# Performance work log

Measured on AMD Instinct MI355X. Metric: run time of the kernel, lower is better.

## Reference

```python
import jax, jax.numpy as jnp
import numpy as np

N_SRC = 100000
N_DST = 20000
N_EDGES = 640000
D_IN = 128
D_OUT = 128


def setup_inputs() -> dict:
    key = jax.random.key(0)
    ks = jax.random.split(key, 6)
    feat_src = jax.random.normal(ks[0], (N_SRC, D_IN), dtype=jnp.float32)
    feat_dst = jax.random.normal(ks[1], (N_DST, D_IN), dtype=jnp.float32)
    src_idx = jax.random.randint(ks[2], (N_EDGES,), 0, N_SRC, dtype=jnp.int64 if jax.config.jax_enable_x64 else jnp.int32)
    dst_idx = jax.random.randint(ks[3], (N_EDGES,), 0, N_DST, dtype=jnp.int64 if jax.config.jax_enable_x64 else jnp.int32)
    # xavier-uniform-ish init scale for [out, in] Linear weights
    lim = float(np.sqrt(6.0 / (D_IN + D_OUT)))
    W_self = jax.random.uniform(ks[4], (D_OUT, D_IN), jnp.float32, -lim, lim)
    W_neigh = jax.random.uniform(ks[5], (D_OUT, D_IN), jnp.float32, -lim, lim)
    b_self = jnp.zeros((D_OUT,), jnp.float32)
    b_neigh = jnp.zeros((D_OUT,), jnp.float32)
    return {
        "feat_src": feat_src, "feat_dst": feat_dst,
        "src_idx": src_idx, "dst_idx": dst_idx,
        "W_self": W_self, "b_self": b_self,
        "W_neigh": W_neigh, "b_neigh": b_neigh,
    }


def reference(feat_src, feat_dst, src_idx, dst_idx, W_self, b_self, W_neigh, b_neigh):
    n_dst = feat_dst.shape[0]
    # message passing: copy_src + mean reduce over incoming edges per dst node
    msgs = feat_src[src_idx]                                   # [E, D_in]
    summed = jax.ops.segment_sum(msgs, dst_idx, num_segments=n_dst)  # [N_dst, D_in]
    deg = jax.ops.segment_sum(jnp.ones((src_idx.shape[0],), feat_src.dtype),
                              dst_idx, num_segments=n_dst)     # [N_dst]
    h_neigh = summed / jnp.maximum(deg, 1.0)[:, None]          # mean (0 for isolated)
    # rst = fc_self(h_self) + fc_neigh(h_neigh); no activation
    rst = (feat_dst @ W_self.T + b_self) + (h_neigh @ W_neigh.T + b_neigh)
    return rst
```

## Files before the change

### kernel.cpp

```cpp
#include <hip/hip_runtime.h>

#define D 128
#define NDST 20000
#define NB 256
#define CAP 96

typedef __attribute__((ext_vector_type(8))) short short8;
typedef __attribute__((ext_vector_type(4))) float f32x4;

__device__ __forceinline__ unsigned f2bf(float f) {
  unsigned x = __float_as_uint(f);
  return (x + 0x7FFFu + ((x >> 16) & 1u)) >> 16;
}
__device__ __forceinline__ unsigned pack2(float a, float b) {
  return f2bf(a) | (f2bf(b) << 16);
}
__device__ __forceinline__ float bflo(unsigned u) { return __uint_as_float(u << 16); }
__device__ __forceinline__ float bfhi(unsigned u) { return __uint_as_float(u & 0xFFFF0000u); }

__global__ __launch_bounds__(512) void p1(
    const int* __restrict__ dst_idx,
    unsigned short* __restrict__ blockHist,
    const float* __restrict__ W_self, const float* __restrict__ W_neigh,
    unsigned short* __restrict__ Wcat,
    unsigned short* __restrict__ fsrc_b,
    int n_src, int n_edges, int EPB)
{
  __shared__ unsigned int hist[NDST];
  const int tid = threadIdx.x;
  const int bid = blockIdx.x;

  if (bid < NB) {
    for (int i = tid; i < NDST / 4; i += 512)
      reinterpret_cast<uint4*>(hist)[i] = make_uint4(0u, 0u, 0u, 0u);
    __syncthreads();
    const int e0 = bid * EPB;
    const int e1 = min(e0 + EPB, n_edges);
    for (int e = e0 + tid; e < e1; e += 512)
      atomicAdd(&hist[dst_idx[e]], 1u);
    __syncthreads();
    unsigned int* rowp =
        reinterpret_cast<unsigned int*>(blockHist + (size_t)bid * NDST);
    for (int i = tid; i < NDST / 2; i += 512) {
      unsigned lo = hist[2 * i], hi = hist[2 * i + 1];
      rowp[i] = (lo & 0xFFFFu) | (hi << 16);
    }
  } else {
    int u = (bid - NB) * 512 + tid;
    const int UW = 32768 / 8;
    if (u < UW) {
      int l = u * 8;
      int n = l >> 8;
      int k0 = l & 255;
      const float* src = (k0 < D) ? (W_self + n * D + k0)
                                  : (W_neigh + n * D + (k0 - D));
      const float4* p = reinterpret_cast<const float4*>(src);
      float4 a = p[0], b = p[1];
      uint4 o;
      o.x = pack2(a.x, a.y); o.y = pack2(a.z, a.w);
      o.z = pack2(b.x, b.y); o.w = pack2(b.z, b.w);
      *reinterpret_cast<uint4*>(Wcat + (size_t)n * 256 + k0) = o;
    } else if (u < UW + D / 8) {
      int q = u - UW;
      *reinterpret_cast<uint4*>(fsrc_b + (size_t)n_src * D + q * 8) =
          make_uint4(0u, 0u, 0u, 0u);
    }
  }
}

__global__ __launch_bounds__(256) void p2conv(
    const float* __restrict__ feat_src,
    unsigned short* __restrict__ fsrc_b,
    unsigned short* __restrict__ blockHist,
    int* __restrict__ degi,
    int n_src, int n_dst, int NPB, int NCB)
{
  const int bid = blockIdx.x;
  const int tid = threadIdx.x;
  if (bid < NPB) {
    int d = bid * 256 + tid;
    if (d < n_dst) {
      unsigned run = 0;
      unsigned short* col = blockHist + d;
      #pragma unroll 8
      for (int b = 0; b < NB; ++b) {
        unsigned h = col[(size_t)b * NDST];
        col[(size_t)b * NDST] = (unsigned short)run;
        run += h;
      }
      degi[d] = (int)run;
    }
  } else {
    const long long NU = (long long)n_src * 16;
    const long long stride = (long long)NCB * 256;
    long long u = (long long)(bid - NPB) * 256 + tid;
    for (; u < NU; u += stride) {
      long long e = u * 8;
      const float4* p = reinterpret_cast<const float4*>(feat_src + e);
      float4 a = p[0], b = p[1];
      uint4 o;
      o.x = pack2(a.x, a.y); o.y = pack2(a.z, a.w);
      o.z = pack2(b.x, b.y); o.w = pack2(b.z, b.w);
      *reinterpret_cast<uint4*>(fsrc_b + e) = o;
    }
  }
}

__global__ __launch_bounds__(512) void p3(
    const int* __restrict__ src_idx,
    const int* __restrict__ dst_idx,
    const unsigned short* __restrict__ blockBase,
    int* __restrict__ bucket,
    int n_edges, int EPB)
{
  __shared__ unsigned int cur[NDST];
  const int tid = threadIdx.x;
  const int bid = blockIdx.x;
  const unsigned int* rowp =
      reinterpret_cast<const unsigned int*>(blockBase + (size_t)bid * NDST);
  for (int i = tid; i < NDST / 2; i += 512) {
    unsigned v = rowp[i];
    cur[2 * i]     = v & 0xFFFFu;
    cur[2 * i + 1] = v >> 16;
  }
  __syncthreads();
  const int e0 = bid * EPB;
  const int e1 = min(e0 + EPB, n_edges);
  for (int e = e0 + tid; e < e1; e += 512) {
    int d = dst_idx[e];
    int s = src_idx[e];
    unsigned r = atomicAdd(&cur[d], 1u);
    if (r < CAP) bucket[(size_t)d * CAP + r] = s;
  }
}

__global__ __launch_bounds__(512) void fused_tail(
    const unsigned short* __restrict__ fsrc_b,
    const int* __restrict__ degi,
    const int* __restrict__ bucket,
    const float* __restrict__ feat_dst,
    const unsigned short* __restrict__ Wcat,
    const float* __restrict__ b_self,
    const float* __restrict__ b_neigh,
    float* __restrict__ out,
    int n_src, int n_dst)
{
  __shared__ unsigned short Af[32][136];
  __shared__ unsigned short Ah[32][136];
  __shared__ unsigned short Bs[128][136];

  const int tid  = threadIdx.x;
  const int w    = tid >> 6;
  const int lane = tid & 63;
  const int row0 = blockIdx.x * 32;

  {
    int r = tid >> 4;
    int q = tid & 15;
    int gr = row0 + r;
    uint4 o = make_uint4(0u, 0u, 0u, 0u);
    if (gr < n_dst) {
      const float4* p = reinterpret_cast<const float4*>(
          feat_dst + (size_t)gr * D + q * 8);
      float4 a = p[0], b = p[1];
      o.x = pack2(a.x, a.y); o.y = pack2(a.z, a.w);
      o.z = pack2(b.x, b.y); o.w = pack2(b.z, b.w);
    }
    *reinterpret_cast<uint4*>(&Af[r][q * 8]) = o;
  }

  {
    const int g = lane >> 4;
    const int c = lane & 15;
    const uint4* fs4 = reinterpret_cast<const uint4*>(fsrc_b);

    for (int it = 0; it < 4; ++it) {
      int row = w * 4 + it;
      int gr = row0 + row;
      if (gr >= n_dst) {
        if (lane < 16)
          *reinterpret_cast<uint4*>(&Ah[row][c * 8]) = make_uint4(0u,0u,0u,0u);
        continue;
      }
      const int total = degi[gr];
      const int use = min(total, CAP);
      const int* brow = bucket + (size_t)gr * CAP;

      float acc[8];
      #pragma unroll
      for (int j = 0; j < 8; ++j) acc[j] = 0.f;

      for (int i = g; i < use; i += 16) {
        int s0 = brow[i];
        int s1 = (i + 4  < use) ? brow[i + 4]  : n_src;
        int s2 = (i + 8  < use) ? brow[i + 8]  : n_src;
        int s3 = (i + 12 < use) ? brow[i + 12] : n_src;
        uint4 v0 = fs4[(size_t)s0 * 16 + c];
        uint4 v1 = fs4[(size_t)s1 * 16 + c];
        uint4 v2 = fs4[(size_t)s2 * 16 + c];
        uint4 v3 = fs4[(size_t)s3 * 16 + c];
        acc[0] += bflo(v0.x); acc[1] += bfhi(v0.x); acc[2] += bflo(v0.y); acc[3] += bfhi(v0.y);
        acc[4] += bflo(v0.z); acc[5] += bfhi(v0.z); acc[6] += bflo(v0.w); acc[7] += bfhi(v0.w);
        acc[0] += bflo(v1.x); acc[1] += bfhi(v1.x); acc[2] += bflo(v1.y); acc[3] += bfhi(v1.y);
        acc[4] += bflo(v1.z); acc[5] += bfhi(v1.z); acc[6] += bflo(v1.w); acc[7] += bfhi(v1.w);
        acc[0] += bflo(v2.x); acc[1] += bfhi(v2.x); acc[2] += bflo(v2.y); acc[3] += bfhi(v2.y);
        acc[4] += bflo(v2.z); acc[5] += bfhi(v2.z); acc[6] += bflo(v2.w); acc[7] += bfhi(v2.w);
        acc[0] += bflo(v3.x); acc[1] += bfhi(v3.x); acc[2] += bflo(v3.y); acc[3] += bfhi(v3.y);
        acc[4] += bflo(v3.z); acc[5] += bfhi(v3.z); acc[6] += bflo(v3.w); acc[7] += bfhi(v3.w);
      }

      #pragma unroll
      for (int j = 0; j < 8; ++j) {
        acc[j] += __shfl_xor(acc[j], 16);
        acc[j] += __shfl_xor(acc[j], 32);
      }

      if (lane < 16) {
        float inv = 1.0f / fmaxf((float)total, 1.0f);
        uint4 o;
        o.x = pack2(acc[0] * inv, acc[1] * inv);
        o.y = pack2(acc[2] * inv, acc[3] * inv);
        o.z = pack2(acc[4] * inv, acc[5] * inv);
        o.w = pack2(acc[6] * inv, acc[7] * inv);
        *reinterpret_cast<uint4*>(&Ah[row][c * 8]) = o;
      }
    }
  }

  const int m  = w & 1;
  const int n0 = (w >> 1) * 2;
  const int ar = m * 16 + (lane & 15);
  const int kb = (lane >> 4) * 8;

  f32x4 acc2[2];
  acc2[0] = (f32x4){0.f, 0.f, 0.f, 0.f};
  acc2[1] = (f32x4){0.f, 0.f, 0.f, 0.f};

  #pragma unroll
  for (int kc = 0; kc < 2; ++kc) {
    __syncthreads();
    {
      int n = tid >> 2;
      int q = tid & 3;
      const uint4* p = reinterpret_cast<const uint4*>(
          Wcat + (size_t)n * 256 + kc * 128 + q * 32);
      uint4 v0 = p[0], v1 = p[1], v2 = p[2], v3 = p[3];
      *reinterpret_cast<uint4*>(&Bs[n][q * 32 + 0])  = v0;
      *reinterpret_cast<uint4*>(&Bs[n][q * 32 + 8])  = v1;
      *reinterpret_cast<uint4*>(&Bs[n][q * 32 + 16]) = v2;
      *reinterpret_cast<uint4*>(&Bs[n][q * 32 + 24]) = v3;
    }
    __syncthreads();

    const unsigned short (*Asrc)[136] = (kc == 0) ? Af : Ah;
    #pragma unroll
    for (int kh = 0; kh < 4; ++kh) {
      short8 a = *reinterpret_cast<const short8*>(&Asrc[ar][kh * 32 + kb]);
      #pragma unroll
      for (int t2 = 0; t2 < 2; ++t2) {
        short8 b = *reinterpret_cast<const short8*>(
            &Bs[(n0 + t2) * 16 + (lane & 15)][kh * 32 + kb]);
        acc2[t2] = __builtin_amdgcn_mfma_f32_16x16x32_bf16(a, b, acc2[t2], 0, 0, 0);
      }
    }
  }

  const int r0 = row0 + m * 16 + (lane >> 4) * 4;
  #pragma unroll
  for (int t2 = 0; t2 < 2; ++t2) {
    int col = (n0 + t2) * 16 + (lane & 15);
    float bv = b_self[col] + b_neigh[col];
    #pragma unroll
    for (int r = 0; r < 4; ++r) {
      int gr = r0 + r;
      if (gr < n_dst) out[(size_t)gr * D + col] = acc2[t2][r] + bv;
    }
  }
}

extern "C" void kernel_launch(void* const* d_in, const int* in_sizes, int n_in,
                              void* d_out, int out_size, void* d_ws, size_t ws_size,
                              hipStream_t stream) {
  const float* feat_src = (const float*)d_in[0];
  const float* feat_dst = (const float*)d_in[1];
  const int*   src_idx  = (const int*)d_in[2];
  const int*   dst_idx  = (const int*)d_in[3];
  const float* W_self   = (const float*)d_in[4];
  const float* b_self   = (const float*)d_in[5];
  const float* W_neigh  = (const float*)d_in[6];
  const float* b_neigh  = (const float*)d_in[7];
  float* out = (float*)d_out;

  const int n_src   = in_sizes[0] / D;
  const int n_dst   = in_sizes[1] / D;
  const int n_edges = in_sizes[2];

  unsigned short* fsrc_b = (unsigned short*)d_ws;
  unsigned short* Wcat   = fsrc_b + (size_t)(n_src + 1) * D;
  int* degi   = (int*)(Wcat + 128 * 256);
  int* bucket = degi + NDST;
  unsigned short* blockHist = (unsigned short*)(bucket + (size_t)NDST * CAP);

  const int EPB = (n_edges + NB - 1) / NB;
  const int extra = (32768 / 8 + D / 8 + 511) / 512;

  p1<<<NB + extra, 512, 0, stream>>>(
      dst_idx, blockHist, W_self, W_neigh, Wcat, fsrc_b, n_src, n_edges, EPB);

  const int NPB = (n_dst + 255) / 256;
  const int NCB = 512;
  p2conv<<<NPB + NCB, 256, 0, stream>>>(
      feat_src, fsrc_b, blockHist, degi, n_src, n_dst, NPB, NCB);

  p3<<<NB, 512, 0, stream>>>(
      src_idx, dst_idx, blockHist, bucket, n_edges, EPB);

  fused_tail<<<(n_dst + 31) / 32, 512, 0, stream>>>(
      fsrc_b, degi, bucket, feat_dst, Wcat, b_self, b_neigh, out,
      n_src, n_dst);
}
```

Baseline: 74.29 us.

## Store gathered source features as FP8 and pack histograms into 16-bit LDS halves

Converts feat_src to FP8 (e4m3) instead of bf16, which halves the bytes gathered per edge in the aggregation kernel. Moves that conversion into the histogram kernel so it overlaps the histogram work, and shrinks the per-block LDS histogram to packed 16-bit counters. Fewer LDS bytes per block may allow more blocks resident. FP8 quantization of activations loses much more precision than bf16 and may exceed the accuracy tolerance.

Measured after the change: 67.30 us. 1.1x faster.

```diff
diff --git a/kernel.cpp b/kernel.cpp
--- a/kernel.cpp
+++ b/kernel.cpp
@@ -7,6 +7,7 @@
 
 typedef __attribute__((ext_vector_type(8))) short short8;
 typedef __attribute__((ext_vector_type(4))) float f32x4;
+typedef __attribute__((ext_vector_type(2))) float f32x2;
 
 __device__ __forceinline__ unsigned f2bf(float f) {
   unsigned x = __float_as_uint(f);
@@ -15,127 +16,121 @@
 __device__ __forceinline__ unsigned pack2(float a, float b) {
   return f2bf(a) | (f2bf(b) << 16);
 }
-__device__ __forceinline__ float bflo(unsigned u) { return __uint_as_float(u << 16); }
-__device__ __forceinline__ float bfhi(unsigned u) { return __uint_as_float(u & 0xFFFF0000u); }
+__device__ __forceinline__ unsigned pack_fp8x4(float a, float b, float c, float d) {
+  int v = 0;
+  v = __builtin_amdgcn_cvt_pk_fp8_f32(a, b, v, false);
+  v = __builtin_amdgcn_cvt_pk_fp8_f32(c, d, v, true);
+  return (unsigned)v;
+}
 
 __global__ __launch_bounds__(512) void p1(
     const int* __restrict__ dst_idx,
-    unsigned short* __restrict__ blockHist,
+    const float* __restrict__ feat_src,
+    unsigned int* __restrict__ blockHist,
+    unsigned char* __restrict__ fsrc8,
     const float* __restrict__ W_self, const float* __restrict__ W_neigh,
     unsigned short* __restrict__ Wcat,
-    unsigned short* __restrict__ fsrc_b,
-    int n_src, int n_edges, int EPB)
+    int n_src, int n_edges, int EPB, int NCB)
 {
-  __shared__ unsigned int hist[NDST];
   const int tid = threadIdx.x;
   const int bid = blockIdx.x;
 
   if (bid < NB) {
-    for (int i = tid; i < NDST / 4; i += 512)
+    __shared__ unsigned int hist[NDST / 2];
+    for (int i = tid; i < NDST / 8; i += 512)
       reinterpret_cast<uint4*>(hist)[i] = make_uint4(0u, 0u, 0u, 0u);
     __syncthreads();
     const int e0 = bid * EPB;
     const int e1 = min(e0 + EPB, n_edges);
-    for (int e = e0 + tid; e < e1; e += 512)
-      atomicAdd(&hist[dst_idx[e]], 1u);
+    for (int e = e0 + tid; e < e1; e += 512) {
+      int d = dst_idx[e];
+      atomicAdd(&hist[d >> 1], 1u << ((d & 1) << 4));
+    }
     __syncthreads();
-    unsigned int* rowp =
-        reinterpret_cast<unsigned int*>(blockHist + (size_t)bid * NDST);
-    for (int i = tid; i < NDST / 2; i += 512) {
-      unsigned lo = hist[2 * i], hi = hist[2 * i + 1];
-      rowp[i] = (lo & 0xFFFFu) | (hi << 16);
-    }
+    uint4* rowp = reinterpret_cast<uint4*>(blockHist + (size_t)bid * (NDST / 2));
+    const uint4* h4 = reinterpret_cast<const uint4*>(hist);
+    for (int i = tid; i < NDST / 8; i += 512) rowp[i] = h4[i];
+  } else if (bid < NB + 8) {
+    int u = (bid - NB) * 512 + tid;
+    int l = u * 8;
+    int n = l >> 8;
+    int k0 = l & 255;
+    const float* src = (k0 < D) ? (W_self + n * D + k0)
+                                : (W_neigh + n * D + (k0 - D));
+    const float4* p = reinterpret_cast<const float4*>(src);
+    float4 a = p[0], b = p[1];
+    uint4 o;
+    o.x = pack2(a.x, a.y); o.y = pack2(a.z, a.w);
+    o.z = pack2(b.x, b.y); o.w = pack2(b.z, b.w);
+    *reinterpret_cast<uint4*>(Wcat + (size_t)n * 256 + k0) = o;
   } else {
-    int u = (bid - NB) * 512 + tid;
-    const int UW = 32768 / 8;
-    if (u < UW) {
-      int l = u * 8;
-      int n = l >> 8;
-      int k0 = l & 255;
-      const float* src = (k0 < D) ? (W_self + n * D + k0)
-                                  : (W_neigh + n * D + (k0 - D));
-      const float4* p = reinterpret_cast<const float4*>(src);
-      float4 a = p[0], b = p[1];
-      uint4 o;
-      o.x = pack2(a.x, a.y); o.y = pack2(a.z, a.w);
-      o.z = pack2(b.x, b.y); o.w = pack2(b.z, b.w);
-      *reinterpret_cast<uint4*>(Wcat + (size_t)n * 256 + k0) = o;
-    } else if (u < UW + D / 8) {
-      int q = u - UW;
-      *reinterpret_cast<uint4*>(fsrc_b + (size_t)n_src * D + q * 8) =
-          make_uint4(0u, 0u, 0u, 0u);
-    }
-  }
-}
-
-__global__ __launch_bounds__(256) void p2conv(
-    const float* __restrict__ feat_src,
-    unsigned short* __restrict__ fsrc_b,
-    unsigned short* __restrict__ blockHist,
+    const long long NCONV = (long long)n_src * 16;
+    const long long NU = NCONV + 16;
+    const long long stride = (long long)NCB * 512;
+    long long u = (long long)(bid - NB - 8) * 512 + tid;
+    for (; u < NU; u += stride) {
+      if (u < NCONV) {
+        long long e = u * 8;
+        const float4* p = reinterpret_cast<const float4*>(feat_src + e);
+        float4 a = p[0], b = p[1];
+        uint2 o;
+        o.x = pack_fp8x4(a.x, a.y, a.z, a.w);
+        o.y = pack_fp8x4(b.x, b.y, b.z, b.w);
+        *reinterpret_cast<uint2*>(fsrc8 + e) = o;
+      } else {
+        *reinterpret_cast<uint2*>(fsrc8 + (size_t)n_src * D + (u - NCONV) * 8) =
+            make_uint2(0u, 0u);
+      }
+    }
+  }
+}
+
+__global__ __launch_bounds__(256) void pB(
+    unsigned int* __restrict__ blockHist,
     int* __restrict__ degi,
-    int n_src, int n_dst, int NPB, int NCB)
+    int n_dst)
 {
-  const int bid = blockIdx.x;
-  const int tid = threadIdx.x;
-  if (bid < NPB) {
-    int d = bid * 256 + tid;
-    if (d < n_dst) {
-      unsigned run = 0;
-      unsigned short* col = blockHist + d;
-      #pragma unroll 8
-      for (int b = 0; b < NB; ++b) {
-        unsigned h = col[(size_t)b * NDST];
-        col[(size_t)b * NDST] = (unsigned short)run;
-        run += h;
-      }
-      degi[d] = (int)run;
-    }
-  } else {
-    const long long NU = (long long)n_src * 16;
-    const long long stride = (long long)NCB * 256;
-    long long u = (long long)(bid - NPB) * 256 + tid;
-    for (; u < NU; u += stride) {
-      long long e = u * 8;
-      const float4* p = reinterpret_cast<const float4*>(feat_src + e);
-      float4 a = p[0], b = p[1];
-      uint4 o;
-      o.x = pack2(a.x, a.y); o.y = pack2(a.z, a.w);
-      o.z = pack2(b.x, b.y); o.w = pack2(b.z, b.w);
-      *reinterpret_cast<uint4*>(fsrc_b + e) = o;
-    }
-  }
+  int d = blockIdx.x * 256 + threadIdx.x;
+  if (d >= n_dst) return;
+  unsigned short* col = reinterpret_cast<unsigned short*>(blockHist) + d;
+  unsigned run = 0;
+  #pragma unroll 8
+  for (int b = 0; b < NB; ++b) {
+    unsigned h = col[(size_t)b * NDST];
+    col[(size_t)b * NDST] = (unsigned short)run;
+    run += h;
+  }
+  degi[d] = (int)run;
 }
 
 __global__ __launch_bounds__(512) void p3(
     const int* __restrict__ src_idx,
     const int* __restrict__ dst_idx,
-    const unsigned short* __restrict__ blockBase,
+    const unsigned int* __restrict__ blockBase,
     int* __restrict__ bucket,
     int n_edges, int EPB)
 {
-  __shared__ unsigned int cur[NDST];
+  __shared__ unsigned int cur[NDST / 2];
   const int tid = threadIdx.x;
   const int bid = blockIdx.x;
-  const unsigned int* rowp =
-      reinterpret_cast<const unsigned int*>(blockBase + (size_t)bid * NDST);
-  for (int i = tid; i < NDST / 2; i += 512) {
-    unsigned v = rowp[i];
-    cur[2 * i]     = v & 0xFFFFu;
-    cur[2 * i + 1] = v >> 16;
-  }
+  const uint4* rowp = reinterpret_cast<const uint4*>(
+      blockBase + (size_t)bid * (NDST / 2));
+  uint4* c4 = reinterpret_cast<uint4*>(cur);
+  for (int i = tid; i < NDST / 8; i += 512) c4[i] = rowp[i];
   __syncthreads();
   const int e0 = bid * EPB;
   const int e1 = min(e0 + EPB, n_edges);
   for (int e = e0 + tid; e < e1; e += 512) {
     int d = dst_idx[e];
     int s = src_idx[e];
-    unsigned r = atomicAdd(&cur[d], 1u);
+    int sh = (d & 1) << 4;
+    unsigned r = (atomicAdd(&cur[d >> 1], 1u << sh) >> sh) & 0xFFFFu;
     if (r < CAP) bucket[(size_t)d * CAP + r] = s;
   }
 }
 
 __global__ __launch_bounds__(512) void fused_tail(
-    const unsigned short* __restrict__ fsrc_b,
+    const unsigned char* __restrict__ fsrc8,
     const int* __restrict__ degi,
     const int* __restrict__ bucket,
     const float* __restrict__ feat_dst,
@@ -172,7 +167,7 @@
   {
     const int g = lane >> 4;
     const int c = lane & 15;
-    const uint4* fs4 = reinterpret_cast<const uint4*>(fsrc_b);
+    const uint2* fs2 = reinterpret_cast<const uint2*>(fsrc8);
 
     for (int it = 0; it < 4; ++it) {
       int row = w * 4 + it;
@@ -195,18 +190,21 @@
         int s1 = (i + 4  < use) ? brow[i + 4]  : n_src;
         int s2 = (i + 8  < use) ? brow[i + 8]  : n_src;
         int s3 = (i + 12 < use) ? brow[i + 12] : n_src;
-        uint4 v0 = fs4[(size_t)s0 * 16 + c];
-        uint4 v1 = fs4[(size_t)s1 * 16 + c];
-        uint4 v2 = fs4[(size_t)s2 * 16 + c];
-        uint4 v3 = fs4[(size_t)s3 * 16 + c];
-        acc[0] += bflo(v0.x); acc[1] += bfhi(v0.x); acc[2] += bflo(v0.y); acc[3] += bfhi(v0.y);
-        acc[4] += bflo(v0.z); acc[5] += bfhi(v0.z); acc[6] += bflo(v0.w); acc[7] += bfhi(v0.w);
-        acc[0] += bflo(v1.x); acc[1] += bfhi(v1.x); acc[2] += bflo(v1.y); acc[3] += bfhi(v1.y);
-        acc[4] += bflo(v1.z); acc[5] += bfhi(v1.z); acc[6] += bflo(v1.w); acc[7] += bfhi(v1.w);
-        acc[0] += bflo(v2.x); acc[1] += bfhi(v2.x); acc[2] += bflo(v2.y); acc[3] += bfhi(v2.y);
-        acc[4] += bflo(v2.z); acc[5] += bfhi(v2.z); acc[6] += bflo(v2.w); acc[7] += bfhi(v2.w);
-        acc[0] += bflo(v3.x); acc[1] += bfhi(v3.x); acc[2] += bflo(v3.y); acc[3] += bfhi(v3.y);
-        acc[4] += bflo(v3.z); acc[5] += bfhi(v3.z); acc[6] += bflo(v3.w); acc[7] += bfhi(v3.w);
+        uint2 v0 = fs2[(size_t)s0 * 16 + c];
+        uint2 v1 = fs2[(size_t)s1 * 16 + c];
+        uint2 v2 = fs2[(size_t)s2 * 16 + c];
+        uint2 v3 = fs2[(size_t)s3 * 16 + c];
+        #pragma unroll
+        for (int k = 0; k < 4; ++k) {
+          unsigned wx = (k == 0) ? v0.x : (k == 1) ? v1.x : (k == 2) ? v2.x : v3.x;
+          unsigned wy = (k == 0) ? v0.y : (k == 1) ? v1.y : (k == 2) ? v2.y : v3.y;
+          f32x2 a0 = __builtin_amdgcn_cvt_pk_f32_fp8(wx, false);
+          f32x2 a1 = __builtin_amdgcn_cvt_pk_f32_fp8(wx, true);
+          f32x2 a2 = __builtin_amdgcn_cvt_pk_f32_fp8(wy, false);
+          f32x2 a3 = __builtin_amdgcn_cvt_pk_f32_fp8(wy, true);
+          acc[0] += a0.x; acc[1] += a0.y; acc[2] += a1.x; acc[3] += a1.y;
+          acc[4] += a2.x; acc[5] += a2.y; acc[6] += a3.x; acc[7] += a3.y;
+        }
       }
 
       #pragma unroll
@@ -295,27 +293,25 @@
   const int n_dst   = in_sizes[1] / D;
   const int n_edges = in_sizes[2];
 
-  unsigned short* fsrc_b = (unsigned short*)d_ws;
-  unsigned short* Wcat   = fsrc_b + (size_t)(n_src + 1) * D;
+  unsigned char* fsrc8 = (unsigned char*)d_ws;
+  unsigned short* Wcat = (unsigned short*)(fsrc8 + (size_t)(n_src + 1) * D);
   int* degi   = (int*)(Wcat + 128 * 256);
   int* bucket = degi + NDST;
-  unsigned short* blockHist = (unsigned short*)(bucket + (size_t)NDST * CAP);
+  unsigned int* blockHist = (unsigned int*)(bucket + (size_t)NDST * CAP);
 
   const int EPB = (n_edges + NB - 1) / NB;
-  const int extra = (32768 / 8 + D / 8 + 511) / 512;
-
-  p1<<<NB + extra, 512, 0, stream>>>(
-      dst_idx, blockHist, W_self, W_neigh, Wcat, fsrc_b, n_src, n_edges, EPB);
-
-  const int NPB = (n_dst + 255) / 256;
-  const int NCB = 512;
-  p2conv<<<NPB + NCB, 256, 0, stream>>>(
-      feat_src, fsrc_b, blockHist, degi, n_src, n_dst, NPB, NCB);
+  const int NCB = 256;
+
+  p1<<<NB + 8 + NCB, 512, 0, stream>>>(
+      dst_idx, feat_src, blockHist, fsrc8, W_self, W_neigh, Wcat,
+      n_src, n_edges, EPB, NCB);
+
+  pB<<<(n_dst + 255) / 256, 256, 0, stream>>>(blockHist, degi, n_dst);
 
   p3<<<NB, 512, 0, stream>>>(
       src_idx, dst_idx, blockHist, bucket, n_edges, EPB);
 
   fused_tail<<<(n_dst + 31) / 32, 512, 0, stream>>>(
-      fsrc_b, degi, bucket, feat_dst, Wcat, b_self, b_neigh, out,
+      fsrc8, degi, bucket, feat_dst, Wcat, b_self, b_neigh, out,
       n_src, n_dst);
 }
```
